# Kernel optimization log

Measured on AMD Instinct MI355X. Metric: run time of the kernel, lower is better.

## Reference

```python
import jax, jax.numpy as jnp
import numpy as np

B, T, W = 8, 4096, 1024          # batch, byte seq len, words per sequence
DB, DW = 64, 512                 # byte_embed_dim, word_embed_dim
NH = 2                           # highway layers per block
VOCAB = 264                      # 256 bytes + 4 + 4 specials
BPE_MARK, WORD_MARK = 4, 3       # bpe_mask_idx, word_mask_idx


def _make_seg_ids():
    # ragged word lengths in {3,4,5}, mean 4, summing to T per sequence
    rng = np.random.default_rng(0)
    seg = np.empty((B, T), np.int32)
    base = T // W
    for b in range(B):
        delta = np.zeros(W, np.int64)
        q = W // 4
        idx = rng.permutation(W)
        delta[idx[:q]] = 1
        delta[idx[q:2 * q]] = -1
        seg[b] = np.repeat(np.arange(W), base + delta)
    return jnp.asarray(seg)


def setup_inputs() -> dict:
    key = jax.random.key(0)
    ks = jax.random.split(key, 12)
    s = 0.05
    byte_tokens = jax.random.randint(ks[0], (B, T), 4, VOCAB)
    bpe_mask = jax.random.bernoulli(ks[1], 0.25, (B, T))
    word_mask = jax.random.bernoulli(ks[2], 0.05, (B, T))
    seg_ids = _make_seg_ids()
    tok_emb = (jax.random.normal(ks[3], (VOCAB, DB)) * s).at[0].set(0.0)  # padding_idx=0 row zeroed
    inp = {
        'byte_tokens': byte_tokens, 'bpe_mask': bpe_mask, 'word_mask': word_mask,
        'seg_ids': seg_ids, 'tok_emb': tok_emb,
        'conv0_w': jax.random.normal(ks[4], (3, DB, DW)) * s, 'conv0_b': jnp.zeros((DW,)),
        'hw0_wg': jax.random.normal(ks[5], (NH, DW, DW)) * s, 'hw0_bg': jnp.zeros((NH, DW)),
        'hw0_wh': jax.random.normal(ks[6], (NH, DW, DW)) * s, 'hw0_bh': jnp.zeros((NH, DW)),
        'conv1_w': jax.random.normal(ks[7], (3, DW, DW)) * s, 'conv1_b': jnp.zeros((DW,)),
        'hw1_wg': jax.random.normal(ks[8], (NH, DW, DW)) * s, 'hw1_bg': jnp.zeros((NH, DW)),
        'hw1_wh': jax.random.normal(ks[9], (NH, DW, DW)) * s, 'hw1_bh': jnp.zeros((NH, DW)),
        'proj_w': jax.random.normal(ks[10], (DW, DW)) * s, 'proj_b': jnp.zeros((DW,)),
    }
    return inp


def _conv_highway(x, cw, cb, wg, bg, wh, bh, residual):
    # 1D same-padded conv over sequence, optional residual, relu, then highways
    y = jax.lax.conv_general_dilated(x, cw, (1,), 'SAME',
                                     dimension_numbers=('NWC', 'WIO', 'NWC')) + cb
    if residual:
        y = y + x
    y = jax.nn.relu(y)
    for i in range(NH):
        g = jax.nn.sigmoid(y @ wg[i] + bg[i])
        h = jax.nn.relu(y @ wh[i] + bh[i])
        y = g * h + (1.0 - g) * y
    return y


def reference(byte_tokens, bpe_mask, word_mask, seg_ids, tok_emb,
              conv0_w, conv0_b, hw0_wg, hw0_bg, hw0_wh, hw0_bh,
              conv1_w, conv1_b, hw1_wg, hw1_bg, hw1_wh, hw1_bh,
              proj_w, proj_b):
    # byte embedding + marker embeddings (pad idx 0 -> zero row)
    x = (tok_emb[byte_tokens]
         + tok_emb[jnp.where(bpe_mask, BPE_MARK, 0)]
         + tok_emb[jnp.where(word_mask, WORD_MARK, 0)])          # [B,T,DB]
    x = _conv_highway(x, conv0_w, conv0_b, hw0_wg, hw0_bg, hw0_wh, hw0_bh, False)
    x = _conv_highway(x, conv1_w, conv1_b, hw1_wg, hw1_bg, hw1_wh, hw1_bh, True)
    # ragged per-word segment max over bytes (fused, replaces python loops)
    seg_max = jax.vmap(lambda xi, si: jax.ops.segment_max(xi, si, num_segments=W))
    x = seg_max(x, seg_ids)                                       # [B,W,DW]
    return x @ proj_w + proj_b
```

## Files before the change

### kernel.cpp

```cpp
#include <hip/hip_runtime.h>
#include <hip/hip_bf16.h>

using bf16 = __hip_bfloat16;
typedef __attribute__((ext_vector_type(8))) short s8v;
typedef __attribute__((ext_vector_type(4))) float f4v;

#define T_SEQ 4096
#define DWC 512

__device__ __forceinline__ float fin(float v) {
    return (v == v && fabsf(v) < 1e30f) ? v : 0.0f;
}
__device__ __forceinline__ float ldf(const void* p, size_t i, int f32) {
    return f32 ? ((const float*)p)[i] : __bfloat162float(((const bf16*)p)[i]);
}
__device__ __forceinline__ float b2f(short s) {
    unsigned u = ((unsigned)(unsigned short)s) << 16;
    return __builtin_bit_cast(float, u);
}
__device__ __forceinline__ short f2b(float v) {
    bf16 b = __float2bfloat16(v);
    return __builtin_bit_cast(short, b);
}
__device__ __forceinline__ uint4 ld16(const short* p) { return *(const uint4*)p; }

__device__ __forceinline__ void swz8(int L, int G, int& bx, int& by) {
    int k8 = L & 7, sl = L >> 3;
    int gp = G >> 6;
    bx = sl & 7;
    by = k8 * gp + (sl >> 3);
}

__device__ __forceinline__ int swidx(int row, int ch) {
    return row * 32 + ((ch ^ ((row >> 1) & 3)) << 3);
}

__global__ __launch_bounds__(256) void diag_kernel(bf16* __restrict__ out, int n, float v)
{
    int i = blockIdx.x * 256 + threadIdx.x;
    if (i < n) out[i] = __float2bfloat16(i == 0 ? v : 0.0f);
}

__global__ __launch_bounds__(256) void detect_kernel(
    const int* __restrict__ tok, const unsigned char* __restrict__ bpe,
    const unsigned char* __restrict__ wm, const int* __restrict__ seg,
    const unsigned int* __restrict__ embw, int* __restrict__ flags)
{
    __shared__ int sh[5];
    int tid = threadIdx.x;
    if (tid < 5) sh[tid] = 0;
    __syncthreads();
    int bo = 0, bm = 0, wo = 0, wmid = 0;
    for (int i = tid; i < 16384; i += 256) {
        int odd = 2 * i + 1;
        if (bpe[odd]) bo = 1;
        if (wm[odd])  wo = 1;
        int mid = 8 * (i & 4095) + 4;
        if (bpe[mid]) bm = 1;
        if (wm[mid])  wmid = 1;
    }
    if (bo)   atomicOr(&sh[0], 1);
    if (bm)   atomicOr(&sh[1], 1);
    if (wo)   atomicOr(&sh[2], 1);
    if (wmid) atomicOr(&sh[3], 1);
    if (tid < 32 && embw[32 + tid] != 0u) atomicOr(&sh[4], 1);
    __syncthreads();
    if (tid == 0) {
        flags[0] = (tok[32767] != 0) ? 0 : 1;
        flags[1] = sh[0] ? 1 : (sh[1] ? 4 : 8);
        flags[2] = sh[2] ? 1 : (sh[3] ? 4 : 8);
        flags[3] = (seg[32767] != 0) ? 0 : 1;
        flags[4] = sh[4] ? 0 : 1;
    }
}

#define WB_TOTAL 3249664
__global__ __launch_bounds__(256) void convert_weights(
    const void* c0w, const void* c0b, const void* h0g, const void* h0bg,
    const void* h0h, const void* h0bh, const void* c1w, const void* c1b,
    const void* h1g, const void* h1bg, const void* h1h, const void* h1bh,
    const void* pw, const void* pb, const int* __restrict__ flags,
    short* __restrict__ WB)
{
    int f32 = flags[4];
    size_t i = (size_t)blockIdx.x * 256 + threadIdx.x;
    if (i >= WB_TOTAL) return;
    const void* src; size_t si;
    if (i < 98304)        { size_t n = i / 192, k = i % 192; src = c0w; si = k * 512 + n; }
    else if (i < 98816)   { src = c0b;  si = i - 98304; }
    else if (i < 623104)  { size_t o = i - 98816;  size_t l = o >> 18; o &= 262143;
                            size_t n = o >> 9, k = o & 511; src = h0g; si = (l << 18) + k * 512 + n; }
    else if (i < 624128)  { src = h0bg; si = i - 623104; }
    else if (i < 1148416) { size_t o = i - 624128; size_t l = o >> 18; o &= 262143;
                            size_t n = o >> 9, k = o & 511; src = h0h; si = (l << 18) + k * 512 + n; }
    else if (i < 1149440) { src = h0bh; si = i - 1148416; }
    else if (i < 1935872) { size_t o = i - 1149440; size_t n = o / 1536, k = o % 1536;
                            src = c1w; si = k * 512 + n; }
    else if (i < 1936384) { src = c1b;  si = i - 1935872; }
    else if (i < 2460672) { size_t o = i - 1936384; size_t l = o >> 18; o &= 262143;
                            size_t n = o >> 9, k = o & 511; src = h1g; si = (l << 18) + k * 512 + n; }
    else if (i < 2461696) { src = h1bg; si = i - 2460672; }
    else if (i < 2985984) { size_t o = i - 2461696; size_t l = o >> 18; o &= 262143;
                            size_t n = o >> 9, k = o & 511; src = h1h; si = (l << 18) + k * 512 + n; }
    else if (i < 2987008) { src = h1bh; si = i - 2985984; }
    else if (i < 3249152) { size_t o = i - 2987008; size_t n = o >> 9, k = o & 511;
                            src = pw; si = k * 512 + n; }
    else                  { src = pb;   si = i - 3249152; }
    WB[i] = f2b(ldf(src, si, f32));
}

__global__ __launch_bounds__(256) void embed_kernel(
    const int* __restrict__ tok, const unsigned char* __restrict__ bpe,
    const unsigned char* __restrict__ wm, const void* __restrict__ emb,
    const int* __restrict__ flags, short* __restrict__ xe, int bt0)
{
    int i = blockIdx.x * 256 + threadIdx.x;
    int d = i & 63;
    int btl = i >> 6;
    int bt = bt0 + btl;
    int is64t = flags[0];
    int wb = flags[1], ww = flags[2];
    int f32 = flags[4];
    int t = is64t ? (int)((const long long*)tok)[bt] : tok[bt];
    t = min(max(t, 0), 263);
    float v = ldf(emb, (size_t)t * 64 + d, f32);
    if (bpe[(size_t)bt * wb]) v += ldf(emb, 4 * 64 + d, f32);
    if (wm[(size_t)bt * ww])  v += ldf(emb, 3 * 64 + d, f32);
    xe[i] = f2b(fin(v));
}

template<int IC, bool RESID>
__global__ __launch_bounds__(256, 4) void conv_mfma(
    const short* __restrict__ A, const short* __restrict__ WT,
    const short* __restrict__ bias, short* __restrict__ Out)
{
    constexpr int K = 3 * IC;
    constexpr int NIT = K / 32;
    __shared__ __align__(16) short As[2][128 * 32];
    __shared__ __align__(16) short Bs[2][64 * 32];
    int bx, by;
    swz8(blockIdx.x, gridDim.x, bx, by);
    const int bm = by * 128, bn = bx * 64;
    const int tid = threadIdx.x;
    const int wave = tid >> 6, lane = tid & 63;
    const int wmr = wave * 32;
    const int q = lane >> 4, ln16 = lane & 15;
    const int srow = tid >> 2, ch = tid & 3;
    const int tt0 = (bm + srow) & (T_SEQ - 1);
    const int tt1 = (bm + srow + 64) & (T_SEQ - 1);

    f4v acc[2][4] = {};
    uint4 rA0, rA1, rB;
    const uint4 z4 = make_uint4(0, 0, 0, 0);

    {
        int t0 = tt0 - 1, t1 = tt1 - 1;
        rA0 = (t0 >= 0 && t0 < T_SEQ) ? ld16(A + (size_t)(bm + srow - 1) * IC + ch * 8) : z4;
        rA1 = (t1 >= 0 && t1 < T_SEQ) ? ld16(A + (size_t)(bm + srow + 63) * IC + ch * 8) : z4;
        rB  = ld16(WT + (size_t)(bn + srow) * K + ch * 8);
    }
    *(uint4*)(&As[0][swidx(srow, ch)])      = rA0;
    *(uint4*)(&As[0][swidx(srow + 64, ch)]) = rA1;
    *(uint4*)(&Bs[0][swidx(srow, ch)])      = rB;
    __syncthreads();
    int p = 0;

    for (int it = 0; it < NIT; ++it) {
        const bool more = (it + 1 < NIT);
        if (more) {
            int kn = (it + 1) * 32;
            int tap = kn / IC, c0 = kn - tap * IC;
            int t0 = tt0 + tap - 1, t1 = tt1 + tap - 1;
            rA0 = (t0 >= 0 && t0 < T_SEQ)
                ? ld16(A + (size_t)(bm + srow + tap - 1) * IC + c0 + ch * 8) : z4;
            rA1 = (t1 >= 0 && t1 < T_SEQ)
                ? ld16(A + (size_t)(bm + srow + 63 + tap) * IC + c0 + ch * 8) : z4;
            rB  = ld16(WT + (size_t)(bn + srow) * K + kn + ch * 8);
        }
        s8v af[2], bf[4];
        #pragma unroll
        for (int mi = 0; mi < 2; mi++) af[mi] = *(const s8v*)(&As[p][swidx(wmr + mi * 16 + ln16, q)]);
        #pragma unroll
        for (int ni = 0; ni < 4; ni++) bf[ni] = *(const s8v*)(&Bs[p][swidx(ni * 16 + ln16, q)]);
        #pragma unroll
        for (int mi = 0; mi < 2; mi++)
            #pragma unroll
            for (int ni = 0; ni < 4; ni++)
                acc[mi][ni] = __builtin_amdgcn_mfma_f32_16x16x32_bf16(
                    af[mi], bf[ni], acc[mi][ni], 0, 0, 0);
        if (more) {
            *(uint4*)(&As[p ^ 1][swidx(srow, ch)])      = rA0;
            *(uint4*)(&As[p ^ 1][swidx(srow + 64, ch)]) = rA1;
            *(uint4*)(&Bs[p ^ 1][swidx(srow, ch)])      = rB;
            __syncthreads();
            p ^= 1;
        }
    }

    #pragma unroll
    for (int mi = 0; mi < 2; mi++)
        #pragma unroll
        for (int ni = 0; ni < 4; ni++) {
            int col = bn + ni * 16 + ln16;
            float bv = b2f(bias[col]);
            #pragma unroll
            for (int r = 0; r < 4; r++) {
                int orow = bm + wmr + mi * 16 + q * 4 + r;
                float v = acc[mi][ni][r] + bv;
                if constexpr (RESID) v += b2f(A[(size_t)orow * IC + col]);
                Out[(size_t)orow * DWC + col] = f2b(fin(fmaxf(v, 0.0f)));
            }
        }
}

__global__ __launch_bounds__(256, 4) void highway_mfma(
    const short* __restrict__ Y, const short* __restrict__ WgT,
    const short* __restrict__ bg, const short* __restrict__ WhT,
    const short* __restrict__ bh, short* __restrict__ Out)
{
    constexpr int NIT = DWC / 32;
    __shared__ __align__(16) short As[2][128 * 32];
    __shared__ __align__(16) short Bg[2][64 * 32];
    __shared__ __align__(16) short Bh[2][64 * 32];
    int bx, by;
    swz8(blockIdx.x, gridDim.x, bx, by);
    const int bm = by * 128, bn = bx * 64;
    const int tid = threadIdx.x;
    const int wave = tid >> 6, lane = tid & 63;
    const int wmr = wave * 32;
    const int q = lane >> 4, ln16 = lane & 15;
    const int srow = tid >> 2, ch = tid & 3;
    const short* A0 = Y   + (size_t)(bm + srow) * DWC + ch * 8;
    const short* A1 = Y   + (size_t)(bm + srow + 64) * DWC + ch * 8;
    const short* G0 = WgT + (size_t)(bn + srow) * DWC + ch * 8;
    const short* H0 = WhT + (size_t)(bn + srow) * DWC + ch * 8;

    f4v accg[2][4] = {};
    f4v acch[2][4] = {};
    uint4 rA0 = ld16(A0), rA1 = ld16(A1), rG = ld16(G0), rH = ld16(H0);
    *(uint4*)(&As[0][swidx(srow, ch)])      = rA0;
    *(uint4*)(&As[0][swidx(srow + 64, ch)]) = rA1;
    *(uint4*)(&Bg[0][swidx(srow, ch)])      = rG;
    *(uint4*)(&Bh[0][swidx(srow, ch)])      = rH;
    __syncthreads();
    int p = 0;

    for (int it = 0; it < NIT; ++it) {
        const bool more = (it + 1 < NIT);
        if (more) {
            int kn = (it + 1) * 32;
            rA0 = ld16(A0 + kn); rA1 = ld16(A1 + kn);
            rG = ld16(G0 + kn);  rH = ld16(H0 + kn);
        }
        s8v af[2], bgf[4], bhf[4];
        #pragma unroll
        for (int mi = 0; mi < 2; mi++) af[mi] = *(const s8v*)(&As[p][swidx(wmr + mi * 16 + ln16, q)]);
        #pragma unroll
        for (int ni = 0; ni < 4; ni++) {
            bgf[ni] = *(const s8v*)(&Bg[p][swidx(ni * 16 + ln16, q)]);
            bhf[ni] = *(const s8v*)(&Bh[p][swidx(ni * 16 + ln16, q)]);
        }
        #pragma unroll
        for (int mi = 0; mi < 2; mi++)
            #pragma unroll
            for (int ni = 0; ni < 4; ni++) {
                accg[mi][ni] = __builtin_amdgcn_mfma_f32_16x16x32_bf16(
                    af[mi], bgf[ni], accg[mi][ni], 0, 0, 0);
                acch[mi][ni] = __builtin_amdgcn_mfma_f32_16x16x32_bf16(
                    af[mi], bhf[ni], acch[mi][ni], 0, 0, 0);
            }
        if (more) {
            *(uint4*)(&As[p ^ 1][swidx(srow, ch)])      = rA0;
            *(uint4*)(&As[p ^ 1][swidx(srow + 64, ch)]) = rA1;
            *(uint4*)(&Bg[p ^ 1][swidx(srow, ch)])      = rG;
            *(uint4*)(&Bh[p ^ 1][swidx(srow, ch)])      = rH;
            __syncthreads();
            p ^= 1;
        }
    }

    #pragma unroll
    for (int mi = 0; mi < 2; mi++)
        #pragma unroll
        for (int ni = 0; ni < 4; ni++) {
            int col = bn + ni * 16 + ln16;
            float bgv = b2f(bg[col]);
            float bhv = b2f(bh[col]);
            #pragma unroll
            for (int r = 0; r < 4; r++) {
                int orow = bm + wmr + mi * 16 + q * 4 + r;
                float g = 1.0f / (1.0f + expf(-(accg[mi][ni][r] + bgv)));
                float h = fmaxf(acch[mi][ni][r] + bhv, 0.0f);
                float y = b2f(Y[(size_t)orow * DWC + col]);
                Out[(size_t)orow * DWC + col] = f2b(fin(g * h + (1.0f - g) * y));
            }
        }
}

__global__ __launch_bounds__(256, 4) void proj_mfma(
    const short* __restrict__ A, const short* __restrict__ WT,
    const short* __restrict__ bias, const int* __restrict__ flags,
    void* __restrict__ Out, int oroff)
{
    constexpr int NIT = DWC / 32;
    __shared__ __align__(16) short As[2][128 * 32];
    __shared__ __align__(16) short Bs[2][64 * 32];
    int bx, by;
    swz8(blockIdx.x, gridDim.x, bx, by);
    const int bm = by * 128, bn = bx * 64;
    const int tid = threadIdx.x;
    const int wave = tid >> 6, lane = tid & 63;
    const int wmr = wave * 32;
    const int q = lane >> 4, ln16 = lane & 15;
    const int srow = tid >> 2, ch = tid & 3;
    const int f32 = flags[4];
    const short* A0 = A  + (size_t)(bm + srow) * DWC + ch * 8;
    const short* A1 = A  + (size_t)(bm + srow + 64) * DWC + ch * 8;
    const short* B0 = WT + (size_t)(bn + srow) * DWC + ch * 8;

    f4v acc[2][4] = {};
    uint4 rA0 = ld16(A0), rA1 = ld16(A1), rB = ld16(B0);
    *(uint4*)(&As[0][swidx(srow, ch)])      = rA0;
    *(uint4*)(&As[0][swidx(srow + 64, ch)]) = rA1;
    *(uint4*)(&Bs[0][swidx(srow, ch)])      = rB;
    __syncthreads();
    int p = 0;

    for (int it = 0; it < NIT; ++it) {
        const bool more = (it + 1 < NIT);
        if (more) {
            int kn = (it + 1) * 32;
            rA0 = ld16(A0 + kn); rA1 = ld16(A1 + kn); rB = ld16(B0 + kn);
        }
        s8v af[2], bf[4];
        #pragma unroll
        for (int mi = 0; mi < 2; mi++) af[mi] = *(const s8v*)(&As[p][swidx(wmr + mi * 16 + ln16, q)]);
        #pragma unroll
        for (int ni = 0; ni < 4; ni++) bf[ni] = *(const s8v*)(&Bs[p][swidx(ni * 16 + ln16, q)]);
        #pragma unroll
        for (int mi = 0; mi < 2; mi++)
            #pragma unroll
            for (int ni = 0; ni < 4; ni++)
                acc[mi][ni] = __builtin_amdgcn_mfma_f32_16x16x32_bf16(
                    af[mi], bf[ni], acc[mi][ni], 0, 0, 0);
        if (more) {
            *(uint4*)(&As[p ^ 1][swidx(srow, ch)])      = rA0;
            *(uint4*)(&As[p ^ 1][swidx(srow + 64, ch)]) = rA1;
            *(uint4*)(&Bs[p ^ 1][swidx(srow, ch)])      = rB;
            __syncthreads();
            p ^= 1;
        }
    }

    #pragma unroll
    for (int mi = 0; mi < 2; mi++)
        #pragma unroll
        for (int ni = 0; ni < 4; ni++) {
            int col = bn + ni * 16 + ln16;
            float bv = b2f(bias[col]);
            #pragma unroll
            for (int r = 0; r < 4; r++) {
                int orow = bm + wmr + mi * 16 + q * 4 + r;
                float v = fin(acc[mi][ni][r] + bv);
                size_t oi = (size_t)(oroff + orow) * DWC + col;
                if (f32) ((float*)Out)[oi] = v;
                else     ((bf16*)Out)[oi] = __float2bfloat16(v);
            }
        }
}

__global__ __launch_bounds__(256) void bounds_kernel(
    const int* __restrict__ seg, const int* __restrict__ flags,
    int* __restrict__ wstart, int* __restrict__ wend, int bt0)
{
    int il = blockIdx.x * 256 + threadIdx.x;
    int ig = bt0 + il;
    int is64 = flags[3];
    const long long* seg64 = (const long long*)seg;
    int t = il & (T_SEQ - 1);
    int bl = il >> 12;
    int s  = (is64 ? (int)seg64[ig] : seg[ig]) & 1023;
    int sp = (t == 0)         ? -1 : ((is64 ? (int)seg64[ig - 1] : seg[ig - 1]) & 1023);
    int sn = (t == T_SEQ - 1) ? -1 : ((is64 ? (int)seg64[ig + 1] : seg[ig + 1]) & 1023);
    int bw = (bl << 10) + s;
    if (sp != s) wstart[bw] = t;
    if (sn != s) wend[bw] = t;
}

__global__ __launch_bounds__(512) void segmax_kernel(
    const short* __restrict__ Y, const int* __restrict__ wstart,
    const int* __restrict__ wend, short* __restrict__ Out)
{
    int bw = blockIdx.x;
    int d = threadIdx.x;
    int bl = bw >> 10;
    int s = wstart[bw], e = wend[bw];
    s = min(max(s, 0), T_SEQ - 1);
    e = min(max(e, s), T_SEQ - 1);
    float m = b2f(Y[(size_t)((bl << 12) + s) * DWC + d]);
    for (int t = s + 1; t <= e; ++t)
        m = fmaxf(m, b2f(Y[(size_t)((bl << 12) + t) * DWC + d]));
    Out[(size_t)bw * DWC + d] = f2b(fin(m));
}

extern "C" void kernel_launch(void* const* d_in, const int* in_sizes, int n_in,
                              void* d_out, int out_size, void* d_ws, size_t ws_size,
                              hipStream_t stream)
{
    static const int expect[19] = {32768, 32768, 32768, 32768, 16896,
                                   98304, 512, 524288, 1024, 524288, 1024,
                                   786432, 512, 524288, 1024, 524288, 1024,
                                   262144, 512};
    int bad = -1;
    if (n_in < 19) bad = 31;
    else for (int i = 0; i < 19; i++) if (in_sizes[i] != expect[i]) { bad = i; break; }
    if (bad >= 0) {
        diag_kernel<<<dim3((out_size + 255) / 256), dim3(256), 0, stream>>>(
            (bf16*)d_out, out_size, 1e35f * (float)(1 + bad));
        return;
    }

    char* ws = (char*)d_ws;
    const size_t WBREG = 8ull << 20;
    short* WB    = (short*)ws;
    int*   flags = (int*)(ws + 6500352);
    const size_t perC = 8921088 + 8192 + 64;
    int C = 8;
    while (C > 1 && WBREG + (size_t)C * perC > ws_size) C >>= 1;
    if (WBREG + (size_t)C * perC > ws_size) {
        float ws_mib = (float)((double)ws_size / 1048576.0);
        diag_kernel<<<dim3((out_size + 255) / 256), dim3(256), 0, stream>>>(
            (bf16*)d_out, out_size, 1e30f * (16.0f + ws_mib));
        return;
    }

    const int*  byte_tokens = (const int*)d_in[0];
    const unsigned char* bpe_mask = (const unsigned char*)d_in[1];
    const unsigned char* word_mask = (const unsigned char*)d_in[2];
    const int*  seg_ids     = (const int*)d_in[3];
    const void* tok_emb = d_in[4];

    detect_kernel<<<dim3(1), dim3(256), 0, stream>>>(
        byte_tokens, bpe_mask, word_mask, seg_ids,
        (const unsigned int*)tok_emb, flags);

    convert_weights<<<dim3((WB_TOTAL + 255) / 256), dim3(256), 0, stream>>>(
        d_in[5], d_in[6], d_in[7], d_in[8], d_in[9], d_in[10],
        d_in[11], d_in[12], d_in[13], d_in[14], d_in[15], d_in[16],
        d_in[17], d_in[18], flags, WB);

    short* c0wT = WB;            short* c0b  = WB + 98304;
    short* h0gT = WB + 98816;    short* h0bg = WB + 623104;
    short* h0hT = WB + 624128;   short* h0bh = WB + 1148416;
    short* c1wT = WB + 1149440;  short* c1b  = WB + 1935872;
    short* h1gT = WB + 1936384;  short* h1bg = WB + 2460672;
    short* h1hT = WB + 2461696;  short* h1bh = WB + 2985984;
    short* pwT  = WB + 2987008;  short* pb   = WB + 3249152;
    const int LOFF = 262144, LBOFF = 512;

    for (int b0 = 0; b0 < 8; b0 += C) {
        const int rows  = C * T_SEQ;
        const int words = C * 1024;
        char*  chunk  = ws + WBREG;
        short* xe     = (short*)chunk;
        short* U      = (short*)(chunk + (size_t)C * 524288);
        short* V      = (short*)(chunk + (size_t)C * (524288 + 4194304));
        int*   wstart = (int*)(chunk + (size_t)C * 8912896);
        int*   wend   = wstart + words;
        short* segout = U;

        embed_kernel<<<dim3(rows * 64 / 256), dim3(256), 0, stream>>>(
            byte_tokens, bpe_mask, word_mask, tok_emb, flags, xe, b0 * T_SEQ);

        dim3 gg(8 * (rows / 128));
        conv_mfma<64, false><<<gg, dim3(256), 0, stream>>>(xe, c0wT, c0b, U);

        highway_mfma<<<gg, dim3(256), 0, stream>>>(U, h0gT, h0bg, h0hT, h0bh, V);
        highway_mfma<<<gg, dim3(256), 0, stream>>>(V, h0gT + LOFF, h0bg + LBOFF,
                                                   h0hT + LOFF, h0bh + LBOFF, U);

        conv_mfma<512, true><<<gg, dim3(256), 0, stream>>>(U, c1wT, c1b, V);

        highway_mfma<<<gg, dim3(256), 0, stream>>>(V, h1gT, h1bg, h1hT, h1bh, U);
        highway_mfma<<<gg, dim3(256), 0, stream>>>(U, h1gT + LOFF, h1bg + LBOFF,
                                                   h1hT + LOFF, h1bh + LBOFF, V);

        bounds_kernel<<<dim3(rows / 256), dim3(256), 0, stream>>>(
            seg_ids, flags, wstart, wend, b0 * T_SEQ);

        segmax_kernel<<<dim3(words), dim3(512), 0, stream>>>(V, wstart, wend, segout);

        proj_mfma<<<dim3(8 * (words / 128)), dim3(256), 0, stream>>>(
            segout, pwT, pb, flags, d_out, b0 * 1024);
    }
}
```

Measured before the change: 492.9 us.

## Load MFMA fragments directly from global memory, dropping LDS staging

The conv, highway and projection GEMM kernels no longer stage A and B tiles through double-buffered shared memory with barriers. Each lane now loads its MFMA operand fragments straight from global memory into registers, prefetching the next k-step into a second register set. This removes the LDS writes, LDS reads and __syncthreads per iteration. In exchange, the weight tiles are loaded once per wave instead of once per block (four times the global/L2 traffic for B), and the loads are short 16-byte per-row strided accesses with no coalesced tile loading. The occupancy hint is also dropped from the launch bounds.

```diff
diff --git a/kernel.cpp b/kernel.cpp
--- a/kernel.cpp
+++ b/kernel.cpp
@@ -22,17 +22,13 @@
     bf16 b = __float2bfloat16(v);
     return __builtin_bit_cast(short, b);
 }
-__device__ __forceinline__ uint4 ld16(const short* p) { return *(const uint4*)p; }
+__device__ __forceinline__ s8v ldfrag(const short* p) { return *(const s8v*)p; }
 
 __device__ __forceinline__ void swz8(int L, int G, int& bx, int& by) {
     int k8 = L & 7, sl = L >> 3;
     int gp = G >> 6;
     bx = sl & 7;
     by = k8 * gp + (sl >> 3);
-}
-
-__device__ __forceinline__ int swidx(int row, int ch) {
-    return row * 32 + ((ch ^ ((row >> 1) & 3)) << 3);
 }
 
 __global__ __launch_bounds__(256) void diag_kernel(bf16* __restrict__ out, int n, float v)
@@ -130,70 +126,68 @@
 }
 
 template<int IC, bool RESID>
-__global__ __launch_bounds__(256, 4) void conv_mfma(
+__global__ __launch_bounds__(256) void conv_mfma(
     const short* __restrict__ A, const short* __restrict__ WT,
     const short* __restrict__ bias, short* __restrict__ Out)
 {
     constexpr int K = 3 * IC;
     constexpr int NIT = K / 32;
-    __shared__ __align__(16) short As[2][128 * 32];
-    __shared__ __align__(16) short Bs[2][64 * 32];
     int bx, by;
     swz8(blockIdx.x, gridDim.x, bx, by);
     const int bm = by * 128, bn = bx * 64;
     const int tid = threadIdx.x;
     const int wave = tid >> 6, lane = tid & 63;
+    const int q = lane >> 4, ln16 = lane & 15;
     const int wmr = wave * 32;
-    const int q = lane >> 4, ln16 = lane & 15;
-    const int srow = tid >> 2, ch = tid & 3;
-    const int tt0 = (bm + srow) & (T_SEQ - 1);
-    const int tt1 = (bm + srow + 64) & (T_SEQ - 1);
+
+    int arow[2], tt[2];
+    #pragma unroll
+    for (int mi = 0; mi < 2; mi++) {
+        arow[mi] = bm + wmr + mi * 16 + ln16;
+        tt[mi] = arow[mi] & (T_SEQ - 1);
+    }
+    const short* Bbase[4];
+    #pragma unroll
+    for (int ni = 0; ni < 4; ni++)
+        Bbase[ni] = WT + (size_t)(bn + ni * 16 + ln16) * K + q * 8;
 
     f4v acc[2][4] = {};
-    uint4 rA0, rA1, rB;
-    const uint4 z4 = make_uint4(0, 0, 0, 0);
-
-    {
-        int t0 = tt0 - 1, t1 = tt1 - 1;
-        rA0 = (t0 >= 0 && t0 < T_SEQ) ? ld16(A + (size_t)(bm + srow - 1) * IC + ch * 8) : z4;
-        rA1 = (t1 >= 0 && t1 < T_SEQ) ? ld16(A + (size_t)(bm + srow + 63) * IC + ch * 8) : z4;
-        rB  = ld16(WT + (size_t)(bn + srow) * K + ch * 8);
-    }
-    *(uint4*)(&As[0][swidx(srow, ch)])      = rA0;
-    *(uint4*)(&As[0][swidx(srow + 64, ch)]) = rA1;
-    *(uint4*)(&Bs[0][swidx(srow, ch)])      = rB;
-    __syncthreads();
-    int p = 0;
+    s8v ca[2], cb[4], na[2], nb[4];
+    const s8v zf = {};
+
+    #pragma unroll
+    for (int mi = 0; mi < 2; mi++) {
+        int ts = tt[mi] - 1;
+        ca[mi] = ((unsigned)ts < T_SEQ) ? ldfrag(A + (size_t)(arow[mi] - 1) * IC + q * 8) : zf;
+    }
+    #pragma unroll
+    for (int ni = 0; ni < 4; ni++) cb[ni] = ldfrag(Bbase[ni]);
 
     for (int it = 0; it < NIT; ++it) {
         const bool more = (it + 1 < NIT);
         if (more) {
             int kn = (it + 1) * 32;
             int tap = kn / IC, c0 = kn - tap * IC;
-            int t0 = tt0 + tap - 1, t1 = tt1 + tap - 1;
-            rA0 = (t0 >= 0 && t0 < T_SEQ)
-                ? ld16(A + (size_t)(bm + srow + tap - 1) * IC + c0 + ch * 8) : z4;
-            rA1 = (t1 >= 0 && t1 < T_SEQ)
-                ? ld16(A + (size_t)(bm + srow + 63 + tap) * IC + c0 + ch * 8) : z4;
-            rB  = ld16(WT + (size_t)(bn + srow) * K + kn + ch * 8);
-        }
-        s8v af[2], bf[4];
-        #pragma unroll
-        for (int mi = 0; mi < 2; mi++) af[mi] = *(const s8v*)(&As[p][swidx(wmr + mi * 16 + ln16, q)]);
-        #pragma unroll
-        for (int ni = 0; ni < 4; ni++) bf[ni] = *(const s8v*)(&Bs[p][swidx(ni * 16 + ln16, q)]);
+            #pragma unroll
+            for (int mi = 0; mi < 2; mi++) {
+                int ts = tt[mi] + tap - 1;
+                na[mi] = ((unsigned)ts < T_SEQ)
+                    ? ldfrag(A + (size_t)(arow[mi] + tap - 1) * IC + c0 + q * 8) : zf;
+            }
+            #pragma unroll
+            for (int ni = 0; ni < 4; ni++) nb[ni] = ldfrag(Bbase[ni] + kn);
+        }
         #pragma unroll
         for (int mi = 0; mi < 2; mi++)
             #pragma unroll
             for (int ni = 0; ni < 4; ni++)
                 acc[mi][ni] = __builtin_amdgcn_mfma_f32_16x16x32_bf16(
-                    af[mi], bf[ni], acc[mi][ni], 0, 0, 0);
-        if (more) {
-            *(uint4*)(&As[p ^ 1][swidx(srow, ch)])      = rA0;
-            *(uint4*)(&As[p ^ 1][swidx(srow + 64, ch)]) = rA1;
-            *(uint4*)(&Bs[p ^ 1][swidx(srow, ch)])      = rB;
-            __syncthreads();
-            p ^= 1;
+                    ca[mi], cb[ni], acc[mi][ni], 0, 0, 0);
+        if (more) {
+            #pragma unroll
+            for (int mi = 0; mi < 2; mi++) ca[mi] = na[mi];
+            #pragma unroll
+            for (int ni = 0; ni < 4; ni++) cb[ni] = nb[ni];
         }
     }
 
@@ -213,69 +207,65 @@
         }
 }
 
-__global__ __launch_bounds__(256, 4) void highway_mfma(
+__global__ __launch_bounds__(256) void highway_mfma(
     const short* __restrict__ Y, const short* __restrict__ WgT,
     const short* __restrict__ bg, const short* __restrict__ WhT,
     const short* __restrict__ bh, short* __restrict__ Out)
 {
     constexpr int NIT = DWC / 32;
-    __shared__ __align__(16) short As[2][128 * 32];
-    __shared__ __align__(16) short Bg[2][64 * 32];
-    __shared__ __align__(16) short Bh[2][64 * 32];
     int bx, by;
     swz8(blockIdx.x, gridDim.x, bx, by);
     const int bm = by * 128, bn = bx * 64;
     const int tid = threadIdx.x;
     const int wave = tid >> 6, lane = tid & 63;
+    const int q = lane >> 4, ln16 = lane & 15;
     const int wmr = wave * 32;
-    const int q = lane >> 4, ln16 = lane & 15;
-    const int srow = tid >> 2, ch = tid & 3;
-    const short* A0 = Y   + (size_t)(bm + srow) * DWC + ch * 8;
-    const short* A1 = Y   + (size_t)(bm + srow + 64) * DWC + ch * 8;
-    const short* G0 = WgT + (size_t)(bn + srow) * DWC + ch * 8;
-    const short* H0 = WhT + (size_t)(bn + srow) * DWC + ch * 8;
+
+    const short* Ab[2];
+    const short* Gb[4];
+    const short* Hb[4];
+    #pragma unroll
+    for (int mi = 0; mi < 2; mi++)
+        Ab[mi] = Y + (size_t)(bm + wmr + mi * 16 + ln16) * DWC + q * 8;
+    #pragma unroll
+    for (int ni = 0; ni < 4; ni++) {
+        size_t ro = (size_t)(bn + ni * 16 + ln16) * DWC + q * 8;
+        Gb[ni] = WgT + ro;
+        Hb[ni] = WhT + ro;
+    }
 
     f4v accg[2][4] = {};
     f4v acch[2][4] = {};
-    uint4 rA0 = ld16(A0), rA1 = ld16(A1), rG = ld16(G0), rH = ld16(H0);
-    *(uint4*)(&As[0][swidx(srow, ch)])      = rA0;
-    *(uint4*)(&As[0][swidx(srow + 64, ch)]) = rA1;
-    *(uint4*)(&Bg[0][swidx(srow, ch)])      = rG;
-    *(uint4*)(&Bh[0][swidx(srow, ch)])      = rH;
-    __syncthreads();
-    int p = 0;
+    s8v ca[2], cg[4], chv[4], na[2], ng[4], nh[4];
+
+    #pragma unroll
+    for (int mi = 0; mi < 2; mi++) ca[mi] = ldfrag(Ab[mi]);
+    #pragma unroll
+    for (int ni = 0; ni < 4; ni++) { cg[ni] = ldfrag(Gb[ni]); chv[ni] = ldfrag(Hb[ni]); }
 
     for (int it = 0; it < NIT; ++it) {
         const bool more = (it + 1 < NIT);
         if (more) {
             int kn = (it + 1) * 32;
-            rA0 = ld16(A0 + kn); rA1 = ld16(A1 + kn);
-            rG = ld16(G0 + kn);  rH = ld16(H0 + kn);
-        }
-        s8v af[2], bgf[4], bhf[4];
-        #pragma unroll
-        for (int mi = 0; mi < 2; mi++) af[mi] = *(const s8v*)(&As[p][swidx(wmr + mi * 16 + ln16, q)]);
-        #pragma unroll
-        for (int ni = 0; ni < 4; ni++) {
-            bgf[ni] = *(const s8v*)(&Bg[p][swidx(ni * 16 + ln16, q)]);
-            bhf[ni] = *(const s8v*)(&Bh[p][swidx(ni * 16 + ln16, q)]);
+            #pragma unroll
+            for (int mi = 0; mi < 2; mi++) na[mi] = ldfrag(Ab[mi] + kn);
+            #pragma unroll
+            for (int ni = 0; ni < 4; ni++) { ng[ni] = ldfrag(Gb[ni] + kn); nh[ni] = ldfrag(Hb[ni] + kn); }
         }
         #pragma unroll
         for (int mi = 0; mi < 2; mi++)
             #pragma unroll
             for (int ni = 0; ni < 4; ni++) {
                 accg[mi][ni] = __builtin_amdgcn_mfma_f32_16x16x32_bf16(
-                    af[mi], bgf[ni], accg[mi][ni], 0, 0, 0);
+                    ca[mi], cg[ni], accg[mi][ni], 0, 0, 0);
                 acch[mi][ni] = __builtin_amdgcn_mfma_f32_16x16x32_bf16(
-                    af[mi], bhf[ni], acch[mi][ni], 0, 0, 0);
+                    ca[mi], chv[ni], acch[mi][ni], 0, 0, 0);
             }
         if (more) {
-            *(uint4*)(&As[p ^ 1][swidx(srow, ch)])      = rA0;
-            *(uint4*)(&As[p ^ 1][swidx(srow + 64, ch)]) = rA1;
-            *(uint4*)(&Bg[p ^ 1][swidx(srow, ch)])      = rG;
-            *(uint4*)(&Bh[p ^ 1][swidx(srow, ch)])      = rH;
-            __syncthreads();
-            p ^= 1;
+            #pragma unroll
+            for (int mi = 0; mi < 2; mi++) ca[mi] = na[mi];
+            #pragma unroll
+            for (int ni = 0; ni < 4; ni++) { cg[ni] = ng[ni]; chv[ni] = nh[ni]; }
         }
     }
 
@@ -297,58 +287,57 @@
         }
 }
 
-__global__ __launch_bounds__(256, 4) void proj_mfma(
+__global__ __launch_bounds__(256) void proj_mfma(
     const short* __restrict__ A, const short* __restrict__ WT,
     const short* __restrict__ bias, const int* __restrict__ flags,
     void* __restrict__ Out, int oroff)
 {
     constexpr int NIT = DWC / 32;
-    __shared__ __align__(16) short As[2][128 * 32];
-    __shared__ __align__(16) short Bs[2][64 * 32];
     int bx, by;
     swz8(blockIdx.x, gridDim.x, bx, by);
     const int bm = by * 128, bn = bx * 64;
     const int tid = threadIdx.x;
     const int wave = tid >> 6, lane = tid & 63;
+    const int q = lane >> 4, ln16 = lane & 15;
     const int wmr = wave * 32;
-    const int q = lane >> 4, ln16 = lane & 15;
-    const int srow = tid >> 2, ch = tid & 3;
     const int f32 = flags[4];
-    const short* A0 = A  + (size_t)(bm + srow) * DWC + ch * 8;
-    const short* A1 = A  + (size_t)(bm + srow + 64) * DWC + ch * 8;
-    const short* B0 = WT + (size_t)(bn + srow) * DWC + ch * 8;
+
+    const short* Ab[2];
+    const short* Bb[4];
+    #pragma unroll
+    for (int mi = 0; mi < 2; mi++)
+        Ab[mi] = A + (size_t)(bm + wmr + mi * 16 + ln16) * DWC + q * 8;
+    #pragma unroll
+    for (int ni = 0; ni < 4; ni++)
+        Bb[ni] = WT + (size_t)(bn + ni * 16 + ln16) * DWC + q * 8;
 
     f4v acc[2][4] = {};
-    uint4 rA0 = ld16(A0), rA1 = ld16(A1), rB = ld16(B0);
-    *(uint4*)(&As[0][swidx(srow, ch)])      = rA0;
-    *(uint4*)(&As[0][swidx(srow + 64, ch)]) = rA1;
-    *(uint4*)(&Bs[0][swidx(srow, ch)])      = rB;
-    __syncthreads();
-    int p = 0;
+    s8v ca[2], cb[4], na[2], nb[4];
+    #pragma unroll
+    for (int mi = 0; mi < 2; mi++) ca[mi] = ldfrag(Ab[mi]);
+    #pragma unroll
+    for (int ni = 0; ni < 4; ni++) cb[ni] = ldfrag(Bb[ni]);
 
     for (int it = 0; it < NIT; ++it) {
         const bool more = (it + 1 < NIT);
         if (more) {
             int kn = (it + 1) * 32;
-            rA0 = ld16(A0 + kn); rA1 = ld16(A1 + kn); rB = ld16(B0 + kn);
-        }
-        s8v af[2], bf[4];
-        #pragma unroll
-        for (int mi = 0; mi < 2; mi++) af[mi] = *(const s8v*)(&As[p][swidx(wmr + mi * 16 + ln16, q)]);
-        #pragma unroll
-        for (int ni = 0; ni < 4; ni++) bf[ni] = *(const s8v*)(&Bs[p][swidx(ni * 16 + ln16, q)]);
+            #pragma unroll
+            for (int mi = 0; mi < 2; mi++) na[mi] = ldfrag(Ab[mi] + kn);
+            #pragma unroll
+            for (int ni = 0; ni < 4; ni++) nb[ni] = ldfrag(Bb[ni] + kn);
+        }
         #pragma unroll
         for (int mi = 0; mi < 2; mi++)
             #pragma unroll
             for (int ni = 0; ni < 4; ni++)
                 acc[mi][ni] = __builtin_amdgcn_mfma_f32_16x16x32_bf16(
-                    af[mi], bf[ni], acc[mi][ni], 0, 0, 0);
-        if (more) {
-            *(uint4*)(&As[p ^ 1][swidx(srow, ch)])      = rA0;
-            *(uint4*)(&As[p ^ 1][swidx(srow + 64, ch)]) = rA1;
-            *(uint4*)(&Bs[p ^ 1][swidx(srow, ch)])      = rB;
-            __syncthreads();
-            p ^= 1;
+                    ca[mi], cb[ni], acc[mi][ni], 0, 0, 0);
+        if (more) {
+            #pragma unroll
+            for (int mi = 0; mi < 2; mi++) ca[mi] = na[mi];
+            #pragma unroll
+            for (int ni = 0; ni < 4; ni++) cb[ni] = nb[ni];
         }
     }
 
```

Result: slower. 1.081 ms (+119.3%).
